# Kernel optimization log

Measured on AMD Instinct MI355X. Metric: run time of the kernel, lower is better.

## Reference

```python
import jax, jax.numpy as jnp
import numpy as np

WS = 8      # window_size
SS = 4      # shift_size
DIM = 64
B, H, W = 4, 256, 256
EPS = 1e-12


def _conv(x, w, groups=1, pad=0):
    return jax.lax.conv_general_dilated(
        x, w, window_strides=(1, 1), padding=[(pad, pad), (pad, pad)],
        feature_group_count=groups,
        dimension_numbers=('NCHW', 'OIHW', 'NCHW'))


def _window_partition(x, ws):
    # Faithful to torch: permute (B,C,nh,ws,nw,ws)->(B,C,nh,nw,ws,ws) then flat view(-1,C,ws,ws)
    b, c, h, w = x.shape
    pb, pr = (-h) % ws, (-w) % ws
    if pb or pr:
        x = jnp.pad(x, ((0, 0), (0, 0), (0, pb), (0, pr)))
    h2, w2 = h + pb, w + pr
    x = x.reshape(b, c, h2 // ws, ws, w2 // ws, ws).transpose(0, 1, 2, 4, 3, 5)
    return x.reshape(-1, c, ws, ws)


def _window_reverse(win, ws, h, w):
    pb, pr = (-h) % ws, (-w) % ws
    h2, w2 = h + pb, w + pr
    b = win.shape[0] * ws * ws // (h2 * w2)
    x = win.reshape(b, -1, h2 // ws, w2 // ws, ws, ws).transpose(0, 1, 2, 4, 3, 5)
    x = x.reshape(b, -1, h2, w2)
    return x[:, :, :h, :w]


def _chan_attn(q, k, v, temp):
    # channel (transposed) attention on flattened window pixels
    n, c = q.shape[0], q.shape[1]
    q = q.reshape(n, c, -1)
    k = k.reshape(n, c, -1)
    v = v.reshape(n, c, -1)
    q = q / jnp.maximum(jnp.linalg.norm(q, axis=-1, keepdims=True), EPS)
    k = k / jnp.maximum(jnp.linalg.norm(k, axis=-1, keepdims=True), EPS)
    attn = jax.nn.softmax(jnp.einsum('ncd,nkd->nck', q, k) / temp, axis=-1)
    out = jnp.einsum('nck,nkd->ncd', attn, v)
    return out.reshape(n, c, WS, WS)


def setup_inputs() -> dict:
    key = jax.random.key(0)
    ks = jax.random.split(key, 10)
    C = DIM
    p = lambda k, s: jax.random.normal(k, s, jnp.float32) * 0.05
    return {
        'x': jax.random.normal(ks[0], (B, C, H, W), jnp.float32),
        'x_f': jax.random.normal(ks[1], (B, C, H, W), jnp.float32),
        'temperature': jnp.ones((1,), jnp.float32),
        'qk_w': p(ks[2], (2 * C, C, 1, 1)),
        'qk_dw_w': p(ks[3], (2 * C, 1, 3, 3)),
        'v_w': p(ks[4], (C, C, 1, 1)),
        'v_dw_w': p(ks[5], (C, 1, 3, 3)),
        'proj_w': p(ks[6], (C, C, 3, 3)),
        'proj1_w': p(ks[7], (C, C, 3, 3)),
        'qkv1_w': p(ks[8], (3 * C, C, 1, 1)),
        'qkv1_dw_w': p(ks[9], (3 * C, 1, 3, 3)),
    }


def reference(x, x_f, temperature, qk_w, qk_dw_w, v_w, v_dw_w,
              proj_w, proj1_w, qkv1_w, qkv1_dw_w):
    b, c, h, w = x.shape
    xw = _window_partition(x, WS)
    xfw = _window_partition(x_f, WS)

    qk = _conv(_conv(xfw, qk_w), qk_dw_w, groups=2 * c, pad=1)
    v = _conv(_conv(xw, v_w), v_dw_w, groups=c, pad=1)
    q, k = jnp.split(qk, 2, axis=1)
    out = _chan_attn(q, k, v, temperature)
    out = _conv(out, proj_w, pad=1)
    out = _window_reverse(out, WS, h, w)

    shift = jnp.roll(out, (-SS, -SS), axis=(2, 3))
    sw = _window_partition(shift, WS)
    qkv = _conv(_conv(sw, qkv1_w), qkv1_dw_w, groups=3 * c, pad=1)
    q, k, v = jnp.split(qkv, 3, axis=1)
    out = _chan_attn(q, k, v, temperature)
    out = _conv(out, proj1_w, pad=1)
    out = _window_reverse(out, WS, h, w)
    out = jnp.roll(out, (SS, SS), axis=(2, 3))
    return out
```

## Files before the change

### kernel.cpp

```cpp
#include <hip/hip_runtime.h>

typedef short v8s __attribute__((ext_vector_type(8)));
typedef float v4f __attribute__((ext_vector_type(4)));
typedef unsigned short u16;

#define MFMA_B16(a, b, c) __builtin_amdgcn_mfma_f32_16x16x32_bf16((a), (b), (c), 0, 0, 0)
#define XS 72

__device__ __forceinline__ u16 bfr(float x) {
    unsigned u = __float_as_uint(x);
    u += 0x7fffu + ((u >> 16) & 1u);
    return (u16)(u >> 16);
}
__device__ __forceinline__ u16 f16r(float x) {
    _Float16 h = (_Float16)x; u16 u; __builtin_memcpy(&u, &h, 2); return u;
}
__device__ __forceinline__ float f16f(u16 u) {
    _Float16 h; __builtin_memcpy(&h, &u, 2); return (float)h;
}

__device__ __forceinline__ void mm_stage(const u16* __restrict__ Ag,
                                         const u16* __restrict__ XB,
                                         u16* __restrict__ M,
                                         int wv, int L, int q)
{
    v4f C[4];
#pragma unroll
    for (int nt = 0; nt < 4; ++nt) C[nt] = (v4f){0.f, 0.f, 0.f, 0.f};
#pragma unroll
    for (int kt = 0; kt < 2; ++kt) {
        v8s a = *(const v8s*)(Ag + (16 * wv + L) * 64 + kt * 32 + q * 8);
#pragma unroll
        for (int nt = 0; nt < 4; ++nt) {
            v8s b = *(const v8s*)(XB + (nt * 16 + L) * XS + kt * 32 + q * 8);
            C[nt] = MFMA_B16(a, b, C[nt]);
        }
    }
    const int rowb = 16 * wv + 4 * q;
#pragma unroll
    for (int r = 0; r < 4; ++r)
#pragma unroll
        for (int nt = 0; nt < 4; ++nt)
            M[(rowb + r) * XS + nt * 16 + L] = f16r(C[nt][r]);
}

__device__ __forceinline__ void dw_read(const u16* __restrict__ M, int c, int r0,
                                        v8s raw[4])
{
#pragma unroll
    for (int r = 0; r < 4; ++r) {
        const int rr = r0 - 1 + r;
        raw[r] = ((unsigned)rr < 8u) ? *(const v8s*)(M + c * XS + rr * 8)
                                     : (v8s){0, 0, 0, 0, 0, 0, 0, 0};
    }
}

template <bool TR, bool NORM>
__device__ __forceinline__ void dw_write(const float* __restrict__ dwg,
                                         const v8s raw[4], int c, int r0,
                                         u16* __restrict__ Out)
{
    float w[9];
#pragma unroll
    for (int k = 0; k < 9; ++k) w[k] = dwg[c * 9 + k];
    float in[4][10];
#pragma unroll
    for (int r = 0; r < 4; ++r) {
        in[r][0] = 0.f; in[r][9] = 0.f;
#pragma unroll
        for (int j = 0; j < 8; ++j) in[r][j + 1] = f16f((u16)raw[r][j]);
    }
    float o[2][8];
#pragma unroll
    for (int rr = 0; rr < 2; ++rr)
#pragma unroll
        for (int j = 0; j < 8; ++j) {
            float s;
            s = w[0] * in[rr][j];
            s = fmaf(w[1], in[rr][j + 1], s);
            s = fmaf(w[2], in[rr][j + 2], s);
            s = fmaf(w[3], in[rr + 1][j], s);
            s = fmaf(w[4], in[rr + 1][j + 1], s);
            s = fmaf(w[5], in[rr + 1][j + 2], s);
            s = fmaf(w[6], in[rr + 2][j], s);
            s = fmaf(w[7], in[rr + 2][j + 1], s);
            s = fmaf(w[8], in[rr + 2][j + 2], s);
            o[rr][j] = s;
        }
    if (NORM) {
        float ss = 0.f;
#pragma unroll
        for (int rr = 0; rr < 2; ++rr)
#pragma unroll
            for (int j = 0; j < 8; ++j) ss = fmaf(o[rr][j], o[rr][j], ss);
        ss += __shfl_xor(ss, 1);
        ss += __shfl_xor(ss, 2);
        const float sc = 1.0f / fmaxf(sqrtf(ss), 1e-12f);
#pragma unroll
        for (int rr = 0; rr < 2; ++rr)
#pragma unroll
            for (int j = 0; j < 8; ++j) o[rr][j] *= sc;
    }
    if (TR) {
#pragma unroll
        for (int rr = 0; rr < 2; ++rr)
#pragma unroll
            for (int j = 0; j < 8; ++j)
                Out[((r0 + rr) * 8 + j) * XS + c] = bfr(o[rr][j]);
    } else {
#pragma unroll
        for (int rr = 0; rr < 2; ++rr) {
            v8s v;
#pragma unroll
            for (int j = 0; j < 8; ++j) v[j] = (short)bfr(o[rr][j]);
            *(v8s*)(Out + c * XS + (r0 + rr) * 8) = v;
        }
    }
}

__device__ __forceinline__ void mm_lds(const u16* __restrict__ Am,
                                       const u16* __restrict__ Bm,
                                       int wv, int L, int q, v4f C[4])
{
#pragma unroll
    for (int nt = 0; nt < 4; ++nt) C[nt] = (v4f){0.f, 0.f, 0.f, 0.f};
#pragma unroll
    for (int kt = 0; kt < 2; ++kt) {
        v8s a = *(const v8s*)(Am + (16 * wv + L) * XS + kt * 32 + q * 8);
#pragma unroll
        for (int nt = 0; nt < 4; ++nt) {
            v8s b = *(const v8s*)(Bm + (nt * 16 + L) * XS + kt * 32 + q * 8);
            C[nt] = MFMA_B16(a, b, C[nt]);
        }
    }
}

__device__ __forceinline__ void proj_mm(const u16* __restrict__ Wg,
                                        const u16* __restrict__ Ot,
                                        int wv, int L, int q, v4f C[4])
{
#pragma unroll
    for (int nt = 0; nt < 4; ++nt) C[nt] = (v4f){0.f, 0.f, 0.f, 0.f};
    const u16* arow = Wg + (16 * wv + L) * 576;
    const int pc = L & 7;
    const int prb = L >> 3;
#pragma unroll
    for (int tap = 0; tap < 9; ++tap) {
        const int dy = tap / 3 - 1, dx = tap % 3 - 1;
        const int spc = pc + dx;
        const bool vc = (unsigned)spc < 8u;
#pragma unroll
        for (int half = 0; half < 2; ++half) {
            v8s a = *(const v8s*)(arow + tap * 64 + half * 32 + q * 8);
#pragma unroll
            for (int nt = 0; nt < 4; ++nt) {
                const int spr = nt * 2 + prb + dy;
                v8s b = {0, 0, 0, 0, 0, 0, 0, 0};
                if (vc && (unsigned)spr < 8u)
                    b = *(const v8s*)(Ot + (spr * 8 + spc) * XS + half * 32 + q * 8);
                C[nt] = MFMA_B16(a, b, C[nt]);
            }
        }
    }
}

__device__ __forceinline__ void softmax_to_lds(v4f S[4], float invt,
                                               u16* __restrict__ Am,
                                               int rowb, int L)
{
#pragma unroll
    for (int nt = 0; nt < 4; ++nt) S[nt] *= invt;
#pragma unroll
    for (int r = 0; r < 4; ++r) {
        float mx = fmaxf(fmaxf(S[0][r], S[1][r]), fmaxf(S[2][r], S[3][r]));
        mx = fmaxf(mx, __shfl_xor(mx, 1));
        mx = fmaxf(mx, __shfl_xor(mx, 2));
        mx = fmaxf(mx, __shfl_xor(mx, 4));
        mx = fmaxf(mx, __shfl_xor(mx, 8));
        float e0 = __expf(S[0][r] - mx);
        float e1 = __expf(S[1][r] - mx);
        float e2 = __expf(S[2][r] - mx);
        float e3 = __expf(S[3][r] - mx);
        float sm = e0 + e1 + e2 + e3;
        sm += __shfl_xor(sm, 1);
        sm += __shfl_xor(sm, 2);
        sm += __shfl_xor(sm, 4);
        sm += __shfl_xor(sm, 8);
        const float ri = 1.0f / sm;
        Am[(rowb + r) * XS + L +  0] = bfr(e0 * ri);
        Am[(rowb + r) * XS + L + 16] = bfr(e1 * ri);
        Am[(rowb + r) * XS + L + 32] = bfr(e2 * ri);
        Am[(rowb + r) * XS + L + 48] = bfr(e3 * ri);
    }
}

__global__ void prep(const float* __restrict__ qk_w, const float* __restrict__ v_w,
                     const float* __restrict__ qkv_w, const float* __restrict__ pw0,
                     const float* __restrict__ pw1, u16* __restrict__ Wb)
{
    int i = blockIdx.x * 256 + threadIdx.x;
    float v;
    if (i < 8192) v = qk_w[i];
    else if (i < 12288) v = v_w[i - 8192];
    else if (i < 24576) v = qkv_w[i - 12288];
    else {
        int j = i - 24576;
        const float* s = pw0;
        if (j >= 36864) { s = pw1; j -= 36864; }
        const int o = j / 576, kk = j % 576;
        const int tap = kk >> 6, c = kk & 63;
        v = s[o * 576 + c * 9 + tap];
    }
    Wb[i] = bfr(v);
}

__global__ __launch_bounds__(256, 4) void k1(
    const float* __restrict__ x, const float* __restrict__ xf,
    const float* __restrict__ temp_p,
    const float* __restrict__ qk_dw, const float* __restrict__ v_dw,
    const u16* __restrict__ Wqk, const u16* __restrict__ Wv,
    const u16* __restrict__ Wp0,
    u16* __restrict__ midb)
{
    __shared__ u16 B0[64 * XS], B1[64 * XS], B2[64 * XS], B3[64 * XS];
    const int t = threadIdx.x, n = blockIdx.x;
    const int lane = t & 63, wv = t >> 6, L = lane & 15, q = lane >> 4;
    const int rowb = 16 * wv + 4 * q;
    const size_t base = (size_t)n << 12;
    const float invt = 1.0f / temp_p[0];
    const int yp = t >> 4, xx0 = (t & 15) << 4;
    const int c2b = (yp >> 3) << 5, ir = (yp & 7) << 3;
    const int dc = t >> 2, dr0 = (t & 3) << 1;

    float4 rx[4];
    {
        const float* sf = xf + base + yp * 256 + xx0;
        const float* sx = x  + base + yp * 256 + xx0;
#pragma unroll
        for (int k = 0; k < 4; ++k) {
            float4 a = *(const float4*)(sf + 4 * k);
            rx[k] = *(const float4*)(sx + 4 * k);
            const int xx = xx0 + 4 * k;
            const int c = c2b + (xx >> 3), pb = ir + (xx & 7);
            B0[(pb + 0) * XS + c] = bfr(a.x);
            B0[(pb + 1) * XS + c] = bfr(a.y);
            B0[(pb + 2) * XS + c] = bfr(a.z);
            B0[(pb + 3) * XS + c] = bfr(a.w);
        }
    }
    __syncthreads();
    mm_stage(Wqk,        B0, B1, wv, L, q);
    mm_stage(Wqk + 4096, B0, B2, wv, L, q);
    __syncthreads();
    {
#pragma unroll
        for (int k = 0; k < 4; ++k) {
            const int xx = xx0 + 4 * k;
            const int c = c2b + (xx >> 3), pb = ir + (xx & 7);
            B3[(pb + 0) * XS + c] = bfr(rx[k].x);
            B3[(pb + 1) * XS + c] = bfr(rx[k].y);
            B3[(pb + 2) * XS + c] = bfr(rx[k].z);
            B3[(pb + 3) * XS + c] = bfr(rx[k].w);
        }
    }
    v8s rawA[4];
    dw_read(B1, dc, dr0, rawA);
    __syncthreads();
    mm_stage(Wv, B3, B0, wv, L, q);
    dw_write<false, true>(qk_dw, rawA, dc, dr0, B1);
    v8s rawB[4];
    dw_read(B2, dc, dr0, rawB);
    __syncthreads();
    dw_write<false, true>(qk_dw + 576, rawB, dc, dr0, B2);
    dw_read(B0, dc, dr0, rawA);
    dw_write<true, false>(v_dw, rawA, dc, dr0, B3);
    __syncthreads();
    v4f S[4];
    mm_lds(B1, B2, wv, L, q, S);
    softmax_to_lds(S, invt, B1, rowb, L);
    __syncthreads();
    v4f O[4];
    mm_lds(B1, B3, wv, L, q, O);
#pragma unroll
    for (int nt = 0; nt < 4; ++nt)
#pragma unroll
        for (int r = 0; r < 4; ++r)
            B2[(L + 16 * nt) * XS + rowb + r] = bfr(O[nt][r]);
    __syncthreads();
    v4f C[4];
    proj_mm(Wp0, B2, wv, L, q, C);
#pragma unroll
    for (int nt = 0; nt < 4; ++nt)
#pragma unroll
        for (int r = 0; r < 4; ++r) {
            const int o = rowb + r, p = L + 16 * nt;
            const int yy = ((o >> 5) << 3) + (p >> 3);
            const int xp = ((o & 31) << 3) + (p & 7);
            midb[base + yy * 256 + xp] = bfr(C[nt][r]);
        }
}

__global__ __launch_bounds__(256, 4) void k2(
    const u16* __restrict__ midb, const float* __restrict__ temp_p,
    const float* __restrict__ qkv_dw,
    const u16* __restrict__ Wqkv, const u16* __restrict__ Wp1,
    float* __restrict__ out)
{
    __shared__ u16 B0[64 * XS], B1[64 * XS], B2[64 * XS], B3[64 * XS];
    const int t = threadIdx.x, m = blockIdx.x;
    const int lane = t & 63, wv = t >> 6, L = lane & 15, q = lane >> 4;
    const int rowb = 16 * wv + 4 * q;
    const int plane = m >> 4, mh2 = m & 15;
    const u16* img = midb + ((size_t)plane << 16);
    const float invt = 1.0f / temp_p[0];
    const int yp = t >> 4, xx0 = (t & 15) << 4;
    const int c2b = (yp >> 3) << 5, ir = (yp & 7) << 3;
    const int dc = t >> 2, dr0 = (t & 3) << 1;

    {
        const int row = (mh2 * 16 + 4 + yp) & 255;
#pragma unroll
        for (int k = 0; k < 4; ++k) {
            const int cc = (xx0 + 4 + 4 * k) & 255;
            ushort4 a = *(const ushort4*)(img + row * 256 + cc);
            const int xx = xx0 + 4 * k;
            const int c = c2b + (xx >> 3), pb = ir + (xx & 7);
            B0[(pb + 0) * XS + c] = a.x;
            B0[(pb + 1) * XS + c] = a.y;
            B0[(pb + 2) * XS + c] = a.z;
            B0[(pb + 3) * XS + c] = a.w;
        }
    }
    __syncthreads();
    mm_stage(Wqkv,        B0, B1, wv, L, q);
    mm_stage(Wqkv + 4096, B0, B2, wv, L, q);
    mm_stage(Wqkv + 8192, B0, B3, wv, L, q);
    __syncthreads();
    v8s rawV[4];
    dw_read(B3, dc, dr0, rawV);
    dw_write<true, false>(qkv_dw + 1152, rawV, dc, dr0, B0);
    v8s rawQ[4];
    dw_read(B1, dc, dr0, rawQ);
    __syncthreads();
    dw_write<false, true>(qkv_dw, rawQ, dc, dr0, B1);
    v8s rawK[4];
    dw_read(B2, dc, dr0, rawK);
    __syncthreads();
    dw_write<false, true>(qkv_dw + 576, rawK, dc, dr0, B2);
    __syncthreads();
    v4f S[4];
    mm_lds(B1, B2, wv, L, q, S);
    softmax_to_lds(S, invt, B1, rowb, L);
    __syncthreads();
    v4f O[4];
    mm_lds(B1, B0, wv, L, q, O);
#pragma unroll
    for (int nt = 0; nt < 4; ++nt)
#pragma unroll
        for (int r = 0; r < 4; ++r)
            B3[(L + 16 * nt) * XS + rowb + r] = bfr(O[nt][r]);
    __syncthreads();
    v4f C[4];
    proj_mm(Wp1, B3, wv, L, q, C);
    float* op = out + ((size_t)plane << 16);
#pragma unroll
    for (int nt = 0; nt < 4; ++nt)
#pragma unroll
        for (int r = 0; r < 4; ++r) {
            const int o = rowb + r, p = L + 16 * nt;
            const int R = mh2 * 16 + ((o >> 5) << 3) + (p >> 3);
            const int orow = (R + 4) & 255;
            const int ocol = ((o & 31) * 8 + (p & 7) + 4) & 255;
            op[orow * 256 + ocol] = C[nt][r];
        }
}

extern "C" void kernel_launch(void* const* d_in, const int* in_sizes, int n_in,
                              void* d_out, int out_size, void* d_ws, size_t ws_size,
                              hipStream_t stream)
{
    const float* x       = (const float*)d_in[0];
    const float* xf      = (const float*)d_in[1];
    const float* temp    = (const float*)d_in[2];
    const float* qk_w    = (const float*)d_in[3];
    const float* qk_dw   = (const float*)d_in[4];
    const float* v_w     = (const float*)d_in[5];
    const float* v_dw    = (const float*)d_in[6];
    const float* proj_w  = (const float*)d_in[7];
    const float* proj1_w = (const float*)d_in[8];
    const float* qkv1_w  = (const float*)d_in[9];
    const float* qkv1_dw = (const float*)d_in[10];
    float* out = (float*)d_out;

    u16* midb = (u16*)d_ws;
    u16* Wb   = (u16*)((char*)d_ws + 33554432);

    prep<<<384, 256, 0, stream>>>(qk_w, v_w, qkv1_w, proj_w, proj1_w, Wb);
    k1<<<4096, 256, 0, stream>>>(x, xf, temp, qk_dw, v_dw,
                                 Wb, Wb + 8192, Wb + 24576, midb);
    k2<<<4096, 256, 0, stream>>>(midb, temp, qkv1_dw,
                                 Wb + 12288, Wb + 61440, out);
}
```

Baseline: 292.5 us.

## Fold depthwise 3x3 into 1x1 weights and compute QKV as MFMA 3x3 convs

Result: slower. 448.6 us (+53.4%).

```diff
diff --git a/kernel.cpp b/kernel.cpp
--- a/kernel.cpp
+++ b/kernel.cpp
@@ -6,114 +6,63 @@
 
 #define MFMA_B16(a, b, c) __builtin_amdgcn_mfma_f32_16x16x32_bf16((a), (b), (c), 0, 0, 0)
 #define XS 72
+#define GROW 64
 
 __device__ __forceinline__ u16 bfr(float x) {
     unsigned u = __float_as_uint(x);
     u += 0x7fffu + ((u >> 16) & 1u);
     return (u16)(u >> 16);
 }
-__device__ __forceinline__ u16 f16r(float x) {
-    _Float16 h = (_Float16)x; u16 u; __builtin_memcpy(&u, &h, 2); return u;
-}
-__device__ __forceinline__ float f16f(u16 u) {
-    _Float16 h; __builtin_memcpy(&h, &u, 2); return (float)h;
-}
-
-__device__ __forceinline__ void mm_stage(const u16* __restrict__ Ag,
-                                         const u16* __restrict__ XB,
-                                         u16* __restrict__ M,
-                                         int wv, int L, int q)
-{
-    v4f C[4];
-#pragma unroll
-    for (int nt = 0; nt < 4; ++nt) C[nt] = (v4f){0.f, 0.f, 0.f, 0.f};
-#pragma unroll
-    for (int kt = 0; kt < 2; ++kt) {
-        v8s a = *(const v8s*)(Ag + (16 * wv + L) * 64 + kt * 32 + q * 8);
-#pragma unroll
-        for (int nt = 0; nt < 4; ++nt) {
-            v8s b = *(const v8s*)(XB + (nt * 16 + L) * XS + kt * 32 + q * 8);
-            C[nt] = MFMA_B16(a, b, C[nt]);
-        }
-    }
-    const int rowb = 16 * wv + 4 * q;
-#pragma unroll
-    for (int r = 0; r < 4; ++r)
-#pragma unroll
-        for (int nt = 0; nt < 4; ++nt)
-            M[(rowb + r) * XS + nt * 16 + L] = f16r(C[nt][r]);
-}
-
-__device__ __forceinline__ void dw_read(const u16* __restrict__ M, int c, int r0,
-                                        v8s raw[4])
-{
-#pragma unroll
-    for (int r = 0; r < 4; ++r) {
-        const int rr = r0 - 1 + r;
-        raw[r] = ((unsigned)rr < 8u) ? *(const v8s*)(M + c * XS + rr * 8)
-                                     : (v8s){0, 0, 0, 0, 0, 0, 0, 0};
-    }
-}
-
-template <bool TR, bool NORM>
-__device__ __forceinline__ void dw_write(const float* __restrict__ dwg,
-                                         const v8s raw[4], int c, int r0,
-                                         u16* __restrict__ Out)
-{
-    float w[9];
-#pragma unroll
-    for (int k = 0; k < 9; ++k) w[k] = dwg[c * 9 + k];
-    float in[4][10];
-#pragma unroll
-    for (int r = 0; r < 4; ++r) {
-        in[r][0] = 0.f; in[r][9] = 0.f;
-#pragma unroll
-        for (int j = 0; j < 8; ++j) in[r][j + 1] = f16f((u16)raw[r][j]);
-    }
-    float o[2][8];
-#pragma unroll
-    for (int rr = 0; rr < 2; ++rr)
-#pragma unroll
-        for (int j = 0; j < 8; ++j) {
-            float s;
-            s = w[0] * in[rr][j];
-            s = fmaf(w[1], in[rr][j + 1], s);
-            s = fmaf(w[2], in[rr][j + 2], s);
-            s = fmaf(w[3], in[rr + 1][j], s);
-            s = fmaf(w[4], in[rr + 1][j + 1], s);
-            s = fmaf(w[5], in[rr + 1][j + 2], s);
-            s = fmaf(w[6], in[rr + 2][j], s);
-            s = fmaf(w[7], in[rr + 2][j + 1], s);
-            s = fmaf(w[8], in[rr + 2][j + 2], s);
-            o[rr][j] = s;
-        }
-    if (NORM) {
-        float ss = 0.f;
-#pragma unroll
-        for (int rr = 0; rr < 2; ++rr)
-#pragma unroll
-            for (int j = 0; j < 8; ++j) ss = fmaf(o[rr][j], o[rr][j], ss);
-        ss += __shfl_xor(ss, 1);
-        ss += __shfl_xor(ss, 2);
-        const float sc = 1.0f / fmaxf(sqrtf(ss), 1e-12f);
-#pragma unroll
-        for (int rr = 0; rr < 2; ++rr)
-#pragma unroll
-            for (int j = 0; j < 8; ++j) o[rr][j] *= sc;
-    }
-    if (TR) {
-#pragma unroll
-        for (int rr = 0; rr < 2; ++rr)
-#pragma unroll
-            for (int j = 0; j < 8; ++j)
-                Out[((r0 + rr) * 8 + j) * XS + c] = bfr(o[rr][j]);
-    } else {
-#pragma unroll
-        for (int rr = 0; rr < 2; ++rr) {
-            v8s v;
-#pragma unroll
-            for (int j = 0; j < 8; ++j) v[j] = (short)bfr(o[rr][j]);
-            *(v8s*)(Out + c * XS + (r0 + rr) * 8) = v;
+
+template <int NA>
+__device__ __forceinline__ void conv_mm(const u16* __restrict__ A0,
+                                        const u16* __restrict__ A1,
+                                        const u16* __restrict__ A2,
+                                        const u16* __restrict__ Xp,
+                                        int wv, int L, int q,
+                                        v4f* __restrict__ C0,
+                                        v4f* __restrict__ C1,
+                                        v4f* __restrict__ C2)
+{
+    const int pc  = L & 7;
+    const int prb = L >> 3;
+#pragma unroll
+    for (int nt = 0; nt < 4; ++nt) {
+        C0[nt] = (v4f){0.f, 0.f, 0.f, 0.f};
+        if (NA > 1) C1[nt] = (v4f){0.f, 0.f, 0.f, 0.f};
+        if (NA > 2) C2[nt] = (v4f){0.f, 0.f, 0.f, 0.f};
+    }
+    const int arow = (16 * wv + L) * 576 + q * 8;
+#pragma unroll
+    for (int dx = -1; dx <= 1; ++dx) {
+        const bool vc = (unsigned)(pc + dx) < 8u;
+        const int cand0 = L + dx - 8;
+#pragma unroll
+        for (int half = 0; half < 2; ++half) {
+            v8s F[9];
+#pragma unroll
+            for (int s = 0; s <= 8; ++s) {
+                const int row = prb + s - 1;
+                const bool ok = vc && ((unsigned)row < 8u);
+                const int idx = ok ? (cand0 + 8 * s) : GROW;
+                F[s] = *(const v8s*)(Xp + idx * XS + half * 32 + q * 8);
+            }
+#pragma unroll
+            for (int dy = -1; dy <= 1; ++dy) {
+                const int tap = (dy + 1) * 3 + (dx + 1);
+                const int ao = arow + tap * 64 + half * 32;
+                v8s a0 = *(const v8s*)(A0 + ao);
+                v8s a1 = a0, a2 = a0;
+                if (NA > 1) a1 = *(const v8s*)(A1 + ao);
+                if (NA > 2) a2 = *(const v8s*)(A2 + ao);
+#pragma unroll
+                for (int nt = 0; nt < 4; ++nt) {
+                    v8s b = F[nt * 2 + dy + 1];
+                    C0[nt] = MFMA_B16(a0, b, C0[nt]);
+                    if (NA > 1) C1[nt] = MFMA_B16(a1, b, C1[nt]);
+                    if (NA > 2) C2[nt] = MFMA_B16(a2, b, C2[nt]);
+                }
+            }
         }
     }
 }
@@ -135,33 +84,32 @@
     }
 }
 
-__device__ __forceinline__ void proj_mm(const u16* __restrict__ Wg,
-                                        const u16* __restrict__ Ot,
-                                        int wv, int L, int q, v4f C[4])
-{
-#pragma unroll
-    for (int nt = 0; nt < 4; ++nt) C[nt] = (v4f){0.f, 0.f, 0.f, 0.f};
-    const u16* arow = Wg + (16 * wv + L) * 576;
-    const int pc = L & 7;
-    const int prb = L >> 3;
-#pragma unroll
-    for (int tap = 0; tap < 9; ++tap) {
-        const int dy = tap / 3 - 1, dx = tap % 3 - 1;
-        const int spc = pc + dx;
-        const bool vc = (unsigned)spc < 8u;
-#pragma unroll
-        for (int half = 0; half < 2; ++half) {
-            v8s a = *(const v8s*)(arow + tap * 64 + half * 32 + q * 8);
-#pragma unroll
-            for (int nt = 0; nt < 4; ++nt) {
-                const int spr = nt * 2 + prb + dy;
-                v8s b = {0, 0, 0, 0, 0, 0, 0, 0};
-                if (vc && (unsigned)spr < 8u)
-                    b = *(const v8s*)(Ot + (spr * 8 + spc) * XS + half * 32 + q * 8);
-                C[nt] = MFMA_B16(a, b, C[nt]);
-            }
-        }
-    }
+__device__ __forceinline__ void norm_write(const v4f C[4], u16* __restrict__ M,
+                                           int rowb, int L)
+{
+#pragma unroll
+    for (int r = 0; r < 4; ++r) {
+        float ss = C[0][r] * C[0][r] + C[1][r] * C[1][r]
+                 + C[2][r] * C[2][r] + C[3][r] * C[3][r];
+        ss += __shfl_xor(ss, 1);
+        ss += __shfl_xor(ss, 2);
+        ss += __shfl_xor(ss, 4);
+        ss += __shfl_xor(ss, 8);
+        const float sc = 1.0f / fmaxf(sqrtf(ss), 1e-12f);
+#pragma unroll
+        for (int nt = 0; nt < 4; ++nt)
+            M[(rowb + r) * XS + L + 16 * nt] = bfr(C[nt][r] * sc);
+    }
+}
+
+__device__ __forceinline__ void tr_write(const v4f C[4], u16* __restrict__ M,
+                                         int rowb, int L)
+{
+#pragma unroll
+    for (int nt = 0; nt < 4; ++nt)
+#pragma unroll
+        for (int r = 0; r < 4; ++r)
+            M[(L + 16 * nt) * XS + rowb + r] = bfr(C[nt][r]);
 }
 
 __device__ __forceinline__ void softmax_to_lds(v4f S[4], float invt,
@@ -194,22 +142,26 @@
     }
 }
 
-__global__ void prep(const float* __restrict__ qk_w, const float* __restrict__ v_w,
-                     const float* __restrict__ qkv_w, const float* __restrict__ pw0,
-                     const float* __restrict__ pw1, u16* __restrict__ Wb)
-{
-    int i = blockIdx.x * 256 + threadIdx.x;
+__global__ void prep(const float* __restrict__ qk_w, const float* __restrict__ qk_dw,
+                     const float* __restrict__ v_w, const float* __restrict__ v_dw,
+                     const float* __restrict__ qkv_w, const float* __restrict__ qkv_dw,
+                     const float* __restrict__ pw0, const float* __restrict__ pw1,
+                     u16* __restrict__ Wb)
+{
+    const int i = blockIdx.x * 256 + threadIdx.x;
+    const int reg = i / 36864, j = i % 36864;
+    const int o = j / 576, kk = j % 576;
+    const int tap = kk >> 6, k = kk & 63;
     float v;
-    if (i < 8192) v = qk_w[i];
-    else if (i < 12288) v = v_w[i - 8192];
-    else if (i < 24576) v = qkv_w[i - 12288];
-    else {
-        int j = i - 24576;
-        const float* s = pw0;
-        if (j >= 36864) { s = pw1; j -= 36864; }
-        const int o = j / 576, kk = j % 576;
-        const int tap = kk >> 6, c = kk & 63;
-        v = s[o * 576 + c * 9 + tap];
+    switch (reg) {
+        case 0: v = qk_dw[o * 9 + tap] * qk_w[o * 64 + k]; break;
+        case 1: v = qk_dw[(o + 64) * 9 + tap] * qk_w[(o + 64) * 64 + k]; break;
+        case 2: v = v_dw[o * 9 + tap] * v_w[o * 64 + k]; break;
+        case 3: v = pw0[o * 576 + k * 9 + tap]; break;
+        case 4: v = qkv_dw[o * 9 + tap] * qkv_w[o * 64 + k]; break;
+        case 5: v = qkv_dw[(o + 64) * 9 + tap] * qkv_w[(o + 64) * 64 + k]; break;
+        case 6: v = qkv_dw[(o + 128) * 9 + tap] * qkv_w[(o + 128) * 64 + k]; break;
+        default: v = pw1[o * 576 + k * 9 + tap]; break;
     }
     Wb[i] = bfr(v);
 }
@@ -217,12 +169,11 @@
 __global__ __launch_bounds__(256, 4) void k1(
     const float* __restrict__ x, const float* __restrict__ xf,
     const float* __restrict__ temp_p,
-    const float* __restrict__ qk_dw, const float* __restrict__ v_dw,
-    const u16* __restrict__ Wqk, const u16* __restrict__ Wv,
-    const u16* __restrict__ Wp0,
+    const u16* __restrict__ Wq, const u16* __restrict__ Wk,
+    const u16* __restrict__ Wv, const u16* __restrict__ Wp,
     u16* __restrict__ midb)
 {
-    __shared__ u16 B0[64 * XS], B1[64 * XS], B2[64 * XS], B3[64 * XS];
+    __shared__ u16 B0[65 * XS], B1[65 * XS], B2[65 * XS], B3[65 * XS];
     const int t = threadIdx.x, n = blockIdx.x;
     const int lane = t & 63, wv = t >> 6, L = lane & 15, q = lane >> 4;
     const int rowb = 16 * wv + 4 * q;
@@ -230,65 +181,44 @@
     const float invt = 1.0f / temp_p[0];
     const int yp = t >> 4, xx0 = (t & 15) << 4;
     const int c2b = (yp >> 3) << 5, ir = (yp & 7) << 3;
-    const int dc = t >> 2, dr0 = (t & 3) << 1;
-
-    float4 rx[4];
+
+    if (t < 64) {
+        B0[GROW * XS + t] = 0; B1[GROW * XS + t] = 0;
+        B2[GROW * XS + t] = 0; B3[GROW * XS + t] = 0;
+    }
     {
         const float* sf = xf + base + yp * 256 + xx0;
         const float* sx = x  + base + yp * 256 + xx0;
 #pragma unroll
         for (int k = 0; k < 4; ++k) {
             float4 a = *(const float4*)(sf + 4 * k);
-            rx[k] = *(const float4*)(sx + 4 * k);
+            float4 b = *(const float4*)(sx + 4 * k);
             const int xx = xx0 + 4 * k;
             const int c = c2b + (xx >> 3), pb = ir + (xx & 7);
-            B0[(pb + 0) * XS + c] = bfr(a.x);
-            B0[(pb + 1) * XS + c] = bfr(a.y);
-            B0[(pb + 2) * XS + c] = bfr(a.z);
-            B0[(pb + 3) * XS + c] = bfr(a.w);
-        }
-    }
-    __syncthreads();
-    mm_stage(Wqk,        B0, B1, wv, L, q);
-    mm_stage(Wqk + 4096, B0, B2, wv, L, q);
-    __syncthreads();
-    {
-#pragma unroll
-        for (int k = 0; k < 4; ++k) {
-            const int xx = xx0 + 4 * k;
-            const int c = c2b + (xx >> 3), pb = ir + (xx & 7);
-            B3[(pb + 0) * XS + c] = bfr(rx[k].x);
-            B3[(pb + 1) * XS + c] = bfr(rx[k].y);
-            B3[(pb + 2) * XS + c] = bfr(rx[k].z);
-            B3[(pb + 3) * XS + c] = bfr(rx[k].w);
-        }
-    }
-    v8s rawA[4];
-    dw_read(B1, dc, dr0, rawA);
-    __syncthreads();
-    mm_stage(Wv, B3, B0, wv, L, q);
-    dw_write<false, true>(qk_dw, rawA, dc, dr0, B1);
-    v8s rawB[4];
-    dw_read(B2, dc, dr0, rawB);
-    __syncthreads();
-    dw_write<false, true>(qk_dw + 576, rawB, dc, dr0, B2);
-    dw_read(B0, dc, dr0, rawA);
-    dw_write<true, false>(v_dw, rawA, dc, dr0, B3);
+            B0[(pb + 0) * XS + c] = bfr(a.x); B0[(pb + 1) * XS + c] = bfr(a.y);
+            B0[(pb + 2) * XS + c] = bfr(a.z); B0[(pb + 3) * XS + c] = bfr(a.w);
+            B3[(pb + 0) * XS + c] = bfr(b.x); B3[(pb + 1) * XS + c] = bfr(b.y);
+            B3[(pb + 2) * XS + c] = bfr(b.z); B3[(pb + 3) * XS + c] = bfr(b.w);
+        }
+    }
+    __syncthreads();
+    v4f CQ[4], CK[4], CV[4], Cd[4];
+    conv_mm<2>(Wq, Wk, nullptr, B0, wv, L, q, CQ, CK, Cd);
+    conv_mm<1>(Wv, nullptr, nullptr, B3, wv, L, q, CV, Cd, Cd);
+    norm_write(CQ, B1, rowb, L);
+    norm_write(CK, B2, rowb, L);
     __syncthreads();
     v4f S[4];
     mm_lds(B1, B2, wv, L, q, S);
-    softmax_to_lds(S, invt, B1, rowb, L);
+    softmax_to_lds(S, invt, B0, rowb, L);
+    tr_write(CV, B3, rowb, L);
     __syncthreads();
     v4f O[4];
-    mm_lds(B1, B3, wv, L, q, O);
-#pragma unroll
-    for (int nt = 0; nt < 4; ++nt)
-#pragma unroll
-        for (int r = 0; r < 4; ++r)
-            B2[(L + 16 * nt) * XS + rowb + r] = bfr(O[nt][r]);
-    __syncthreads();
-    v4f C[4];
-    proj_mm(Wp0, B2, wv, L, q, C);
+    mm_lds(B0, B3, wv, L, q, O);
+    tr_write(O, B1, rowb, L);
+    __syncthreads();
+    v4f CP[4];
+    conv_mm<1>(Wp, nullptr, nullptr, B1, wv, L, q, CP, Cd, Cd);
 #pragma unroll
     for (int nt = 0; nt < 4; ++nt)
 #pragma unroll
@@ -296,28 +226,31 @@
             const int o = rowb + r, p = L + 16 * nt;
             const int yy = ((o >> 5) << 3) + (p >> 3);
             const int xp = ((o & 31) << 3) + (p & 7);
-            midb[base + yy * 256 + xp] = bfr(C[nt][r]);
+            midb[base + yy * 256 + xp] = bfr(CP[nt][r]);
         }
 }
 
 __global__ __launch_bounds__(256, 4) void k2(
     const u16* __restrict__ midb, const float* __restrict__ temp_p,
-    const float* __restrict__ qkv_dw,
-    const u16* __restrict__ Wqkv, const u16* __restrict__ Wp1,
+    const u16* __restrict__ Wq, const u16* __restrict__ Wk,
+    const u16* __restrict__ Wv, const u16* __restrict__ Wp,
     float* __restrict__ out)
 {
-    __shared__ u16 B0[64 * XS], B1[64 * XS], B2[64 * XS], B3[64 * XS];
+    __shared__ u16 B0[65 * XS], B1[65 * XS], B2[65 * XS], B3[65 * XS];
     const int t = threadIdx.x, m = blockIdx.x;
     const int lane = t & 63, wv = t >> 6, L = lane & 15, q = lane >> 4;
     const int rowb = 16 * wv + 4 * q;
     const int plane = m >> 4, mh2 = m & 15;
     const u16* img = midb + ((size_t)plane << 16);
     const float invt = 1.0f / temp_p[0];
-    const int yp = t >> 4, xx0 = (t & 15) << 4;
-    const int c2b = (yp >> 3) << 5, ir = (yp & 7) << 3;
-    const int dc = t >> 2, dr0 = (t & 3) << 1;
-
+
+    if (t < 64) {
+        B0[GROW * XS + t] = 0; B1[GROW * XS + t] = 0;
+        B2[GROW * XS + t] = 0; B3[GROW * XS + t] = 0;
+    }
     {
+        const int yp = t >> 4, xx0 = (t & 15) << 4;
+        const int c2b = (yp >> 3) << 5, ir = (yp & 7) << 3;
         const int row = (mh2 * 16 + 4 + yp) & 255;
 #pragma unroll
         for (int k = 0; k < 4; ++k) {
@@ -332,36 +265,22 @@
         }
     }
     __syncthreads();
-    mm_stage(Wqkv,        B0, B1, wv, L, q);
-    mm_stage(Wqkv + 4096, B0, B2, wv, L, q);
-    mm_stage(Wqkv + 8192, B0, B3, wv, L, q);
-    __syncthreads();
-    v8s rawV[4];
-    dw_read(B3, dc, dr0, rawV);
-    dw_write<true, false>(qkv_dw + 1152, rawV, dc, dr0, B0);
-    v8s rawQ[4];
-    dw_read(B1, dc, dr0, rawQ);
-    __syncthreads();
-    dw_write<false, true>(qkv_dw, rawQ, dc, dr0, B1);
-    v8s rawK[4];
-    dw_read(B2, dc, dr0, rawK);
-    __syncthreads();
-    dw_write<false, true>(qkv_dw + 576, rawK, dc, dr0, B2);
+    v4f CQ[4], CK[4], CV[4], Cd[4];
+    conv_mm<3>(Wq, Wk, Wv, B0, wv, L, q, CQ, CK, CV);
+    norm_write(CQ, B1, rowb, L);
+    norm_write(CK, B2, rowb, L);
+    tr_write(CV, B3, rowb, L);
     __syncthreads();
     v4f S[4];
     mm_lds(B1, B2, wv, L, q, S);
-    softmax_to_lds(S, invt, B1, rowb, L);
+    softmax_to_lds(S, invt, B0, rowb, L);
     __syncthreads();
     v4f O[4];
-    mm_lds(B1, B0, wv, L, q, O);
-#pragma unroll
-    for (int nt = 0; nt < 4; ++nt)
-#pragma unroll
-        for (int r = 0; r < 4; ++r)
-            B3[(L + 16 * nt) * XS + rowb + r] = bfr(O[nt][r]);
-    __syncthreads();
-    v4f C[4];
-    proj_mm(Wp1, B3, wv, L, q, C);
+    mm_lds(B0, B3, wv, L, q, O);
+    tr_write(O, B1, rowb, L);
+    __syncthreads();
+    v4f CP[4];
+    conv_mm<1>(Wp, nullptr, nullptr, B1, wv, L, q, CP, Cd, Cd);
     float* op = out + ((size_t)plane << 16);
 #pragma unroll
     for (int nt = 0; nt < 4; ++nt)
@@ -371,7 +290,7 @@
             const int R = mh2 * 16 + ((o >> 5) << 3) + (p >> 3);
             const int orow = (R + 4) & 255;
             const int ocol = ((o & 31) * 8 + (p & 7) + 4) & 255;
-            op[orow * 256 + ocol] = C[nt][r];
+            op[orow * 256 + ocol] = CP[nt][r];
         }
 }
 
@@ -395,9 +314,11 @@
     u16* midb = (u16*)d_ws;
     u16* Wb   = (u16*)((char*)d_ws + 33554432);
 
-    prep<<<384, 256, 0, stream>>>(qk_w, v_w, qkv1_w, proj_w, proj1_w, Wb);
-    k1<<<4096, 256, 0, stream>>>(x, xf, temp, qk_dw, v_dw,
-                                 Wb, Wb + 8192, Wb + 24576, midb);
-    k2<<<4096, 256, 0, stream>>>(midb, temp, qkv1_dw,
-                                 Wb + 12288, Wb + 61440, out);
-}
+    prep<<<1152, 256, 0, stream>>>(qk_w, qk_dw, v_w, v_dw, qkv1_w, qkv1_dw,
+                                   proj_w, proj1_w, Wb);
+    k1<<<4096, 256, 0, stream>>>(x, xf, temp,
+                                 Wb, Wb + 36864, Wb + 73728, Wb + 110592, midb);
+    k2<<<4096, 256, 0, stream>>>(midb, temp,
+                                 Wb + 147456, Wb + 184320, Wb + 221184, Wb + 258048,
+                                 out);
+}
```
